# Performance work log

Measured on AMD Instinct MI355X. Metric: run time of the kernel, lower is better.

Reference implementation:

```python
import jax, jax.numpy as jnp
import numpy as np

IN_F = 1024
OUT_F = 1024
N_ORDER = 13  # grid_size=10 + spline_order=3
RMS_EPS = 1e-6


def setup_inputs() -> dict:
    key = jax.random.key(0)
    k_x, k_b, k_p = jax.random.split(key, 3)
    x = jax.random.normal(k_x, (4, 2048, IN_F), dtype=jnp.float32)
    # flax param init: normal(stddev=scale_base/sqrt(in_features)) etc.
    base_weight = jax.random.normal(k_b, (IN_F, OUT_F), dtype=jnp.float32) * (1.0 / np.sqrt(IN_F))
    poly_weight = jax.random.normal(k_p, (N_ORDER, IN_F, OUT_F), dtype=jnp.float32) * (0.1 / np.sqrt(IN_F * N_ORDER))
    rms_scale = jnp.ones((OUT_F,), dtype=jnp.float32)  # nn.RMSNorm default scale init
    return {"x": x, "base_weight": base_weight, "poly_weight": poly_weight, "rms_scale": rms_scale}


def reference(x, base_weight, poly_weight, rms_scale):
    orig_dtype = x.dtype
    prefix = x.shape[:-1]
    x_2d = x.reshape(-1, IN_F)  # [B, in]

    # Base path: SiLU(x) @ W_base in bf16
    x_c = x_2d.astype(jnp.bfloat16)
    out = jax.nn.silu(x_c) @ base_weight.astype(jnp.bfloat16)  # [B, out] bf16

    # Chebyshev recursion on tanh-normalized fp32 input
    x_safe = jnp.tanh(x_2d.astype(jnp.float32))
    pw = poly_weight.astype(jnp.bfloat16)
    T_prev = jnp.ones_like(x_safe)
    T_curr = x_safe
    out = out + T_prev.astype(jnp.bfloat16) @ pw[0]
    out = out + T_curr.astype(jnp.bfloat16) @ pw[1]
    for k in range(2, N_ORDER):  # fixed small unroll (13 orders)
        T_next = 2.0 * x_safe * T_curr - T_prev
        out = out + T_next.astype(jnp.bfloat16) @ pw[k]
        T_prev = T_curr
        T_curr = T_next

    # RMSNorm (flax default: eps=1e-6, learned scale)
    o32 = out.astype(jnp.float32)
    ms = jnp.mean(o32 * o32, axis=-1, keepdims=True)
    o32 = o32 * jax.lax.rsqrt(ms + RMS_EPS) * rms_scale
    return o32.astype(orig_dtype).reshape(prefix + (OUT_F,))
```

## Files before the change

kernel.cpp:

```cpp
#include <hip/hip_runtime.h>
#include <cstdint>

#define IN_F  1024
#define OUT_F 1024
#define NORD  13
#define BROWS 8192

typedef __bf16 bf16x8 __attribute__((ext_vector_type(8)));
typedef float  f32x4  __attribute__((ext_vector_type(4)));
typedef unsigned short u16x8 __attribute__((ext_vector_type(8)));
typedef unsigned short u16x4 __attribute__((ext_vector_type(4)));

__device__ __forceinline__ unsigned short f2bf(float f) {
  unsigned int u = __float_as_uint(f);
  unsigned int r = u + 0x7FFFu + ((u >> 16) & 1u);
  return (unsigned short)(r >> 16);
}
__device__ __forceinline__ float bf2f(unsigned short h) {
  return __uint_as_float(((unsigned int)h) << 16);
}
__device__ __forceinline__ float bfround(float f) { return bf2f(f2bf(f)); }

__device__ __forceinline__ void gload_lds16(const void* g, void* l) {
  __builtin_amdgcn_global_load_lds(
      (__attribute__((address_space(1))) unsigned int*)(uintptr_t)g,
      (__attribute__((address_space(3))) unsigned int*)(unsigned int)(uintptr_t)l,
      16, 0, 0);
}

__global__ __launch_bounds__(256)
void act_kernel(const float* __restrict__ x, unsigned short* __restrict__ A,
                int b0, int nb, int Kp) {
  int t   = threadIdx.x;
  int row = blockIdx.x * 2 + (t >> 7);
  int f0  = (t & 127) * 8;
  const float* xr = x + (size_t)row * IN_F + f0;
  float xv[8];
  *(float4*)&xv[0] = *(const float4*)&xr[0];
  *(float4*)&xv[4] = *(const float4*)&xr[4];
  unsigned short* Ar = A + (size_t)row * Kp;
  int omax = b0 + nb - 1;
  if (b0 == 0) {
    u16x8 sv;
#pragma unroll
    for (int i = 0; i < 8; i++) {
      float xc = bfround(xv[i]);
      float sg = bfround(1.0f / (1.0f + expf(-xc)));
      sv[i] = f2bf(xc * sg);
    }
    *(u16x8*)&Ar[f0] = sv;
  }
  float xs[8], tp[8], tc[8];
#pragma unroll
  for (int i = 0; i < 8; i++) { xs[i] = tanhf(xv[i]); tp[i] = 1.0f; tc[i] = xs[i]; }
  for (int o = 1; o <= omax; o++) {
    if (o >= b0) {
      int bb = o - b0;
      u16x8 sv;
#pragma unroll
      for (int i = 0; i < 8; i++) sv[i] = f2bf(tc[i]);
      *(u16x8*)&Ar[(size_t)bb * 1024 + f0] = sv;
    }
    {
#pragma clang fp contract(off)
#pragma unroll
      for (int i = 0; i < 8; i++) {
        float tm = 2.0f * xs[i] * tc[i];
        float tn = tm - tp[i];
        tp[i] = tc[i]; tc[i] = tn;
      }
    }
  }
}

__global__ __launch_bounds__(256)
void wprep_kernel(const float* __restrict__ baseW, const float* __restrict__ poly,
                  unsigned short* __restrict__ Wt, int b0, int Kp) {
  __shared__ float tile[64][65];
  int bb = blockIdx.z;
  int g  = b0 + bb;
  const float* src = (g == 0) ? baseW : (poly + (size_t)g * (IN_F * OUT_F));
  int n0 = blockIdx.x * 64, f0 = blockIdx.y * 64;
  int tx = threadIdx.x, ty = threadIdx.y;
#pragma unroll
  for (int i = 0; i < 16; i++)
    tile[ty + i * 4][tx] = src[(size_t)(f0 + ty + i * 4) * OUT_F + n0 + tx];
  __syncthreads();
#pragma unroll
  for (int i = 0; i < 16; i++)
    Wt[(size_t)(n0 + ty + i * 4) * Kp + (size_t)bb * 1024 + f0 + tx] = f2bf(tile[tx][ty + i * 4]);
}

__global__ __launch_bounds__(256)
void bias1_kernel(const float* __restrict__ pw0, float* __restrict__ partial) {
  int t  = threadIdx.x;
  int n  = blockIdx.x * 256 + t;
  int fc = blockIdx.y;
  float s = 0.f;
  for (int f = fc * 128; f < fc * 128 + 128; f++)
    s += bf2f(f2bf(pw0[(size_t)f * OUT_F + n]));
  partial[(size_t)fc * OUT_F + n] = s;
}
__global__ __launch_bounds__(256)
void bias2_kernel(const float* __restrict__ partial, float* __restrict__ bias) {
  int n = blockIdx.x * 256 + threadIdx.x;
  float s = 0.f;
#pragma unroll
  for (int fc = 0; fc < 8; fc++) s += partial[(size_t)fc * OUT_F + n];
  bias[n] = s;
}

__global__ __launch_bounds__(256, 2)
void gemm_kernel(const unsigned short* __restrict__ A, const unsigned short* __restrict__ Wt,
                 unsigned short* __restrict__ outAcc, const float* __restrict__ bias,
                 int Kp, int isFirst) {
  __shared__ unsigned short sA[2][128 * 64];
  __shared__ unsigned short sB[2][128 * 64];
  int t    = threadIdx.x;
  int m0   = blockIdx.x * 128;
  int n0   = blockIdx.y * 128;
  int wave = t >> 6, lane = t & 63;
  int lr   = lane & 15, quad = lane >> 4;
  int wm   = (wave & 1) * 64, wn = (wave >> 1) * 64;

  int rs = t >> 3;
  int jg = (t & 7) ^ (rs & 7);
  const unsigned short* aSrc = A  + (size_t)(m0 + rs) * Kp + jg * 8;
  const unsigned short* bSrc = Wt + (size_t)(n0 + rs) * Kp + jg * 8;
  char* sAc = (char*)sA;
  char* sBc = (char*)sB;
  int ldsOff = t * 16;

  int aOff[4][2], bOff[4][2];
#pragma unroll
  for (int mi = 0; mi < 4; mi++) {
    int row = wm + mi * 16 + lr;
#pragma unroll
    for (int ks = 0; ks < 2; ks++) {
      int j = ks * 4 + quad;
      aOff[mi][ks] = row * 128 + ((j ^ (row & 7)) * 16);
    }
  }
#pragma unroll
  for (int ni = 0; ni < 4; ni++) {
    int row = wn + ni * 16 + lr;
#pragma unroll
    for (int ks = 0; ks < 2; ks++) {
      int j = ks * 4 + quad;
      bOff[ni][ks] = row * 128 + ((j ^ (row & 7)) * 16);
    }
  }

  f32x4 s[4][4];
  float bsr[4];
  if (isFirst) {
#pragma unroll
    for (int ni = 0; ni < 4; ni++) bsr[ni] = bfround(bias[n0 + wn + ni * 16 + lr]);
  } else {
#pragma unroll
    for (int ni = 0; ni < 4; ni++) {
      int gn = n0 + wn + ni * 16 + lr;
#pragma unroll
      for (int mi = 0; mi < 4; mi++) {
        int gmBase = m0 + wm + mi * 16 + quad * 4;
#pragma unroll
        for (int r = 0; r < 4; r++)
          s[mi][ni][r] = bf2f(outAcc[(size_t)(gmBase + r) * OUT_F + gn]);
      }
    }
  }

  int nKt  = Kp >> 6;
  int nBlk = Kp >> 10;

  auto stage = [&](int gkt, int buf) {
    const unsigned short* aP = aSrc + gkt * 64;
    const unsigned short* bP = bSrc + gkt * 64;
    char* dA = sAc + buf * 16384 + ldsOff;
    char* dB = sBc + buf * 16384 + ldsOff;
#pragma unroll
    for (int rd = 0; rd < 4; rd++)
      gload_lds16(aP + (size_t)rd * 32 * Kp, dA + rd * 4096);
#pragma unroll
    for (int rd = 0; rd < 4; rd++)
      gload_lds16(bP + (size_t)rd * 32 * Kp, dB + rd * 4096);
  };

  stage(0, 0);

  int gkt = 0;
  for (int blk = 0; blk < nBlk; blk++) {
    f32x4 acc[4][4];
#pragma unroll
    for (int mi = 0; mi < 4; mi++)
#pragma unroll
      for (int ni = 0; ni < 4; ni++)
        acc[mi][ni] = (f32x4){0.f, 0.f, 0.f, 0.f};

    for (int kt = 0; kt < 16; kt++, gkt++) {
      __syncthreads();
      int nxt = gkt + 1;
      if (nxt < nKt) stage(nxt, nxt & 1);
      int buf = gkt & 1;
      char* bA = sAc + buf * 16384;
      char* bB = sBc + buf * 16384;
#pragma unroll
      for (int ks = 0; ks < 2; ks++) {
        bf16x8 af[4], bfr[4];
#pragma unroll
        for (int mi = 0; mi < 4; mi++) af[mi] = *(const bf16x8*)(bA + aOff[mi][ks]);
#pragma unroll
        for (int ni = 0; ni < 4; ni++) bfr[ni] = *(const bf16x8*)(bB + bOff[ni][ks]);
#pragma unroll
        for (int mi = 0; mi < 4; mi++)
#pragma unroll
          for (int ni = 0; ni < 4; ni++)
            acc[mi][ni] = __builtin_amdgcn_mfma_f32_16x16x32_bf16(af[mi], bfr[ni], acc[mi][ni], 0, 0, 0);
      }
    }

    bool firstBlk = (isFirst && blk == 0);
    if (firstBlk) {
#pragma unroll
      for (int mi = 0; mi < 4; mi++)
#pragma unroll
        for (int ni = 0; ni < 4; ni++)
#pragma unroll
          for (int r = 0; r < 4; r++) {
            float p = bfround(acc[mi][ni][r]);
            s[mi][ni][r] = bfround(p + bsr[ni]);
          }
    } else {
#pragma unroll
      for (int mi = 0; mi < 4; mi++)
#pragma unroll
        for (int ni = 0; ni < 4; ni++)
#pragma unroll
          for (int r = 0; r < 4; r++)
            s[mi][ni][r] = bfround(s[mi][ni][r] + bfround(acc[mi][ni][r]));
    }
  }

#pragma unroll
  for (int ni = 0; ni < 4; ni++) {
    int gn = n0 + wn + ni * 16 + lr;
#pragma unroll
    for (int mi = 0; mi < 4; mi++) {
      int gmBase = m0 + wm + mi * 16 + quad * 4;
#pragma unroll
      for (int r = 0; r < 4; r++)
        outAcc[(size_t)(gmBase + r) * OUT_F + gn] = f2bf(s[mi][ni][r]);
    }
  }
}

__global__ __launch_bounds__(256)
void rms_kernel(const unsigned short* __restrict__ outAcc, const float* __restrict__ scale,
                float* __restrict__ out) {
  int row = blockIdx.x;
  int t   = threadIdx.x;
  const unsigned short* src = outAcc + (size_t)row * OUT_F;
  u16x4 hv = *(const u16x4*)&src[t * 4];
  float v[4];
#pragma unroll
  for (int i = 0; i < 4; i++) v[i] = bf2f(hv[i]);
  float s = v[0]*v[0] + v[1]*v[1] + v[2]*v[2] + v[3]*v[3];
#pragma unroll
  for (int off = 32; off > 0; off >>= 1) s += __shfl_down(s, off, 64);
  __shared__ float red[4];
  if ((t & 63) == 0) red[t >> 6] = s;
  __syncthreads();
  float tot = red[0] + red[1] + red[2] + red[3];
  float sc = 1.0f / sqrtf(tot * (1.0f / OUT_F) + 1e-6f);
  float4 so = *(const float4*)&scale[t * 4];
  float4 o;
  o.x = v[0] * sc * so.x; o.y = v[1] * sc * so.y;
  o.z = v[2] * sc * so.z; o.w = v[3] * sc * so.w;
  *(float4*)&out[(size_t)row * OUT_F + t * 4] = o;
}

extern "C" void kernel_launch(void* const* d_in, const int* in_sizes, int n_in,
                              void* d_out, int out_size, void* d_ws, size_t ws_size,
                              hipStream_t stream) {
  const float* x     = (const float*)d_in[0];
  const float* baseW = (const float*)d_in[1];
  const float* poly  = (const float*)d_in[2];
  const float* scale = (const float*)d_in[3];
  float* out = (float*)d_out;

  char* ws = (char*)d_ws;
  unsigned short* outAcc = (unsigned short*)ws;
  float* bias    = (float*)(ws + 16777216);
  float* partial = (float*)(ws + 16777216 + 4096);
  size_t fixed   = 16777216 + 4096 + 32768;

  int CHB = 1;
  for (int c = NORD; c >= 1; c--) {
    size_t need = fixed + (size_t)c * 1024 * OUT_F * 2
                + (size_t)BROWS * c * 1024 * 2;
    if (need <= ws_size) { CHB = c; break; }
  }
  unsigned short* Wt = (unsigned short*)(ws + fixed);
  unsigned short* Ap = (unsigned short*)(ws + fixed + (size_t)CHB * 1024 * OUT_F * 2);

  bias1_kernel<<<dim3(4, 8), 256, 0, stream>>>(poly, partial);
  bias2_kernel<<<4, 256, 0, stream>>>(partial, bias);

  for (int b0 = 0; b0 < NORD; b0 += CHB) {
    int nb = (CHB < NORD - b0) ? CHB : (NORD - b0);
    int Kp = nb * 1024;
    act_kernel<<<BROWS / 2, 256, 0, stream>>>(x, Ap, b0, nb, Kp);
    wprep_kernel<<<dim3(16, 16, nb), dim3(64, 4), 0, stream>>>(baseW, poly, Wt, b0, Kp);
    gemm_kernel<<<dim3(BROWS / 128, 8), 256, 0, stream>>>(Ap, Wt, outAcc, bias, Kp, (b0 == 0) ? 1 : 0);
  }
  rms_kernel<<<BROWS, 256, 0, stream>>>(outAcc, scale, out);
}
```

Measured before the change: 407.0 us.

## Prefetch two K-tiles ahead with explicit vmcnt waits and swap to fast tanh/exp

```diff
diff --git a/kernel.cpp b/kernel.cpp
--- a/kernel.cpp
+++ b/kernel.cpp
@@ -20,6 +20,11 @@
   return __uint_as_float(((unsigned int)h) << 16);
 }
 __device__ __forceinline__ float bfround(float f) { return bf2f(f2bf(f)); }
+
+__device__ __forceinline__ float fast_tanh(float x) {
+  float e = __expf(2.0f * x);
+  return 1.0f - 2.0f / (e + 1.0f);
+}
 
 __device__ __forceinline__ void gload_lds16(const void* g, void* l) {
   __builtin_amdgcn_global_load_lds(
@@ -45,14 +50,14 @@
 #pragma unroll
     for (int i = 0; i < 8; i++) {
       float xc = bfround(xv[i]);
-      float sg = bfround(1.0f / (1.0f + expf(-xc)));
+      float sg = bfround(1.0f / (1.0f + __expf(-xc)));
       sv[i] = f2bf(xc * sg);
     }
     *(u16x8*)&Ar[f0] = sv;
   }
   float xs[8], tp[8], tc[8];
 #pragma unroll
-  for (int i = 0; i < 8; i++) { xs[i] = tanhf(xv[i]); tp[i] = 1.0f; tc[i] = xs[i]; }
+  for (int i = 0; i < 8; i++) { xs[i] = fast_tanh(xv[i]); tp[i] = 1.0f; tc[i] = xs[i]; }
   for (int o = 1; o <= omax; o++) {
     if (o >= b0) {
       int bb = o - b0;
@@ -187,8 +192,10 @@
   };
 
   stage(0, 0);
-
-  int gkt = 0;
+  stage(1, 1);
+
+  int gkt   = 0;
+  int nKtm1 = nKt - 1;
   for (int blk = 0; blk < nBlk; blk++) {
     f32x4 acc[4][4];
 #pragma unroll
@@ -198,25 +205,39 @@
         acc[mi][ni] = (f32x4){0.f, 0.f, 0.f, 0.f};
 
     for (int kt = 0; kt < 16; kt++, gkt++) {
-      __syncthreads();
-      int nxt = gkt + 1;
-      if (nxt < nKt) stage(nxt, nxt & 1);
+      if (gkt != nKtm1) {
+        asm volatile("s_waitcnt vmcnt(8)" ::: "memory");
+      } else {
+        asm volatile("s_waitcnt vmcnt(0)" ::: "memory");
+      }
+      __builtin_amdgcn_s_barrier();
+      __builtin_amdgcn_sched_barrier(0);
+
       int buf = gkt & 1;
       char* bA = sAc + buf * 16384;
       char* bB = sBc + buf * 16384;
+      bf16x8 af[2][4], bfr[2][4];
 #pragma unroll
       for (int ks = 0; ks < 2; ks++) {
-        bf16x8 af[4], bfr[4];
-#pragma unroll
-        for (int mi = 0; mi < 4; mi++) af[mi] = *(const bf16x8*)(bA + aOff[mi][ks]);
-#pragma unroll
-        for (int ni = 0; ni < 4; ni++) bfr[ni] = *(const bf16x8*)(bB + bOff[ni][ks]);
+#pragma unroll
+        for (int mi = 0; mi < 4; mi++) af[ks][mi] = *(const bf16x8*)(bA + aOff[mi][ks]);
+#pragma unroll
+        for (int ni = 0; ni < 4; ni++) bfr[ks][ni] = *(const bf16x8*)(bB + bOff[ni][ks]);
+      }
+      asm volatile("s_waitcnt lgkmcnt(0)" ::: "memory");
+      __builtin_amdgcn_s_barrier();
+      __builtin_amdgcn_sched_barrier(0);
+
+      int nxt = gkt + 2;
+      if (nxt < nKt) stage(nxt, buf);
+
+#pragma unroll
+      for (int ks = 0; ks < 2; ks++)
 #pragma unroll
         for (int mi = 0; mi < 4; mi++)
 #pragma unroll
           for (int ni = 0; ni < 4; ni++)
-            acc[mi][ni] = __builtin_amdgcn_mfma_f32_16x16x32_bf16(af[mi], bfr[ni], acc[mi][ni], 0, 0, 0);
-      }
+            acc[mi][ni] = __builtin_amdgcn_mfma_f32_16x16x32_bf16(af[ks][mi], bfr[ks][ni], acc[mi][ni], 0, 0, 0);
     }
 
     bool firstBlk = (isFirst && blk == 0);
```

Result: slower. 431.9 us (+6.1%).

## Load GEMM A operand directly into registers, drop A LDS staging; fast tanh

Applied to the files above, without the earlier changes.

```diff
diff --git a/kernel.cpp b/kernel.cpp
--- a/kernel.cpp
+++ b/kernel.cpp
@@ -20,6 +20,11 @@
   return __uint_as_float(((unsigned int)h) << 16);
 }
 __device__ __forceinline__ float bfround(float f) { return bf2f(f2bf(f)); }
+
+__device__ __forceinline__ float fast_tanh(float x) {
+  float e = __expf(2.0f * x);
+  return 1.0f - 2.0f / (e + 1.0f);
+}
 
 __device__ __forceinline__ void gload_lds16(const void* g, void* l) {
   __builtin_amdgcn_global_load_lds(
@@ -45,14 +50,17 @@
 #pragma unroll
     for (int i = 0; i < 8; i++) {
       float xc = bfround(xv[i]);
-      float sg = bfround(1.0f / (1.0f + expf(-xc)));
+      float sg = bfround(1.0f / (1.0f + __expf(-xc)));
       sv[i] = f2bf(xc * sg);
     }
     *(u16x8*)&Ar[f0] = sv;
   }
-  float xs[8], tp[8], tc[8];
-#pragma unroll
-  for (int i = 0; i < 8; i++) { xs[i] = tanhf(xv[i]); tp[i] = 1.0f; tc[i] = xs[i]; }
+  float xs2[8], tp[8], tc[8];
+#pragma unroll
+  for (int i = 0; i < 8; i++) {
+    float xs = fast_tanh(xv[i]);
+    tp[i] = 1.0f; tc[i] = xs; xs2[i] = xs + xs;
+  }
   for (int o = 1; o <= omax; o++) {
     if (o >= b0) {
       int bb = o - b0;
@@ -65,7 +73,7 @@
 #pragma clang fp contract(off)
 #pragma unroll
       for (int i = 0; i < 8; i++) {
-        float tm = 2.0f * xs[i] * tc[i];
+        float tm = xs2[i] * tc[i];
         float tn = tm - tp[i];
         tp[i] = tc[i]; tc[i] = tn;
       }
@@ -114,7 +122,6 @@
 void gemm_kernel(const unsigned short* __restrict__ A, const unsigned short* __restrict__ Wt,
                  unsigned short* __restrict__ outAcc, const float* __restrict__ bias,
                  int Kp, int isFirst) {
-  __shared__ unsigned short sA[2][128 * 64];
   __shared__ unsigned short sB[2][128 * 64];
   int t    = threadIdx.x;
   int m0   = blockIdx.x * 128;
@@ -125,22 +132,11 @@
 
   int rs = t >> 3;
   int jg = (t & 7) ^ (rs & 7);
-  const unsigned short* aSrc = A  + (size_t)(m0 + rs) * Kp + jg * 8;
   const unsigned short* bSrc = Wt + (size_t)(n0 + rs) * Kp + jg * 8;
-  char* sAc = (char*)sA;
   char* sBc = (char*)sB;
   int ldsOff = t * 16;
 
-  int aOff[4][2], bOff[4][2];
-#pragma unroll
-  for (int mi = 0; mi < 4; mi++) {
-    int row = wm + mi * 16 + lr;
-#pragma unroll
-    for (int ks = 0; ks < 2; ks++) {
-      int j = ks * 4 + quad;
-      aOff[mi][ks] = row * 128 + ((j ^ (row & 7)) * 16);
-    }
-  }
+  int bOff[4][2];
 #pragma unroll
   for (int ni = 0; ni < 4; ni++) {
     int row = wn + ni * 16 + lr;
@@ -151,7 +147,9 @@
     }
   }
 
-  f32x4 s[4][4];
+  const unsigned short* aBase = A + (size_t)(m0 + wm + lr) * Kp + quad * 8;
+
+  unsigned short sp[4][4][4];
   float bsr[4];
   if (isFirst) {
 #pragma unroll
@@ -165,7 +163,7 @@
         int gmBase = m0 + wm + mi * 16 + quad * 4;
 #pragma unroll
         for (int r = 0; r < 4; r++)
-          s[mi][ni][r] = bf2f(outAcc[(size_t)(gmBase + r) * OUT_F + gn]);
+          sp[mi][ni][r] = outAcc[(size_t)(gmBase + r) * OUT_F + gn];
       }
     }
   }
@@ -173,50 +171,66 @@
   int nKt  = Kp >> 6;
   int nBlk = Kp >> 10;
 
-  auto stage = [&](int gkt, int buf) {
-    const unsigned short* aP = aSrc + gkt * 64;
+  auto stageB = [&](int gkt, int buf) {
     const unsigned short* bP = bSrc + gkt * 64;
-    char* dA = sAc + buf * 16384 + ldsOff;
     char* dB = sBc + buf * 16384 + ldsOff;
-#pragma unroll
-    for (int rd = 0; rd < 4; rd++)
-      gload_lds16(aP + (size_t)rd * 32 * Kp, dA + rd * 4096);
 #pragma unroll
     for (int rd = 0; rd < 4; rd++)
       gload_lds16(bP + (size_t)rd * 32 * Kp, dB + rd * 4096);
   };
 
-  stage(0, 0);
-
+  auto loadA = [&](int gkt, bf16x8 (&ar)[4][2]) {
+    const unsigned short* p = aBase + (size_t)gkt * 64;
+#pragma unroll
+    for (int mi = 0; mi < 4; mi++)
+#pragma unroll
+      for (int ks = 0; ks < 2; ks++)
+        ar[mi][ks] = *(const bf16x8*)(p + (size_t)mi * 16 * Kp + ks * 32);
+  };
+
+  bf16x8 arP[4][2], arQ[4][2];
+
+  stageB(0, 0);
+  loadA(0, arP);
+
+  f32x4 acc[4][4];
   int gkt = 0;
+
+  auto ktStep = [&](const bf16x8 (&arC)[4][2], bf16x8 (&arN)[4][2]) {
+    __syncthreads();
+    int nxt = gkt + 1;
+    int buf = gkt & 1;
+    if (nxt < nKt) {
+      stageB(nxt, buf ^ 1);
+      loadA(nxt, arN);
+    }
+    char* bB = sBc + buf * 16384;
+    bf16x8 bfv[2][4];
+#pragma unroll
+    for (int ks = 0; ks < 2; ks++)
+#pragma unroll
+      for (int ni = 0; ni < 4; ni++)
+        bfv[ks][ni] = *(const bf16x8*)(bB + bOff[ni][ks]);
+#pragma unroll
+    for (int ks = 0; ks < 2; ks++)
+#pragma unroll
+      for (int mi = 0; mi < 4; mi++)
+#pragma unroll
+        for (int ni = 0; ni < 4; ni++)
+          acc[mi][ni] = __builtin_amdgcn_mfma_f32_16x16x32_bf16(arC[mi][ks], bfv[ks][ni], acc[mi][ni], 0, 0, 0);
+    gkt++;
+  };
+
   for (int blk = 0; blk < nBlk; blk++) {
-    f32x4 acc[4][4];
 #pragma unroll
     for (int mi = 0; mi < 4; mi++)
 #pragma unroll
       for (int ni = 0; ni < 4; ni++)
         acc[mi][ni] = (f32x4){0.f, 0.f, 0.f, 0.f};
 
-    for (int kt = 0; kt < 16; kt++, gkt++) {
-      __syncthreads();
-      int nxt = gkt + 1;
-      if (nxt < nKt) stage(nxt, nxt & 1);
-      int buf = gkt & 1;
-      char* bA = sAc + buf * 16384;
-      char* bB = sBc + buf * 16384;
-#pragma unroll
-      for (int ks = 0; ks < 2; ks++) {
-        bf16x8 af[4], bfr[4];
-#pragma unroll
-        for (int mi = 0; mi < 4; mi++) af[mi] = *(const bf16x8*)(bA + aOff[mi][ks]);
-#pragma unroll
-        for (int ni = 0; ni < 4; ni++) bfr[ni] = *(const bf16x8*)(bB + bOff[ni][ks]);
-#pragma unroll
-        for (int mi = 0; mi < 4; mi++)
-#pragma unroll
-          for (int ni = 0; ni < 4; ni++)
-            acc[mi][ni] = __builtin_amdgcn_mfma_f32_16x16x32_bf16(af[mi], bfr[ni], acc[mi][ni], 0, 0, 0);
-      }
+    for (int kt2 = 0; kt2 < 8; kt2++) {
+      ktStep(arP, arQ);
+      ktStep(arQ, arP);
     }
 
     bool firstBlk = (isFirst && blk == 0);
@@ -228,7 +242,7 @@
 #pragma unroll
           for (int r = 0; r < 4; r++) {
             float p = bfround(acc[mi][ni][r]);
-            s[mi][ni][r] = bfround(p + bsr[ni]);
+            sp[mi][ni][r] = f2bf(p + bsr[ni]);
           }
     } else {
 #pragma unroll
@@ -237,7 +251,7 @@
         for (int ni = 0; ni < 4; ni++)
 #pragma unroll
           for (int r = 0; r < 4; r++)
-            s[mi][ni][r] = bfround(s[mi][ni][r] + bfround(acc[mi][ni][r]));
+            sp[mi][ni][r] = f2bf(bf2f(sp[mi][ni][r]) + bfround(acc[mi][ni][r]));
     }
   }
 
@@ -249,7 +263,7 @@
       int gmBase = m0 + wm + mi * 16 + quad * 4;
 #pragma unroll
       for (int r = 0; r < 4; r++)
-        outAcc[(size_t)(gmBase + r) * OUT_F + gn] = f2bf(s[mi][ni][r]);
+        outAcc[(size_t)(gmBase + r) * OUT_F + gn] = sp[mi][ni][r];
     }
   }
 }
```

New measurement: 621.6 us. +52.7%, slower.

## Use two-wave GEMM blocks with larger per-wave tiles and fast tanh/exp

Applied to the files above, without the earlier changes.

```diff
diff --git a/kernel.cpp b/kernel.cpp
--- a/kernel.cpp
+++ b/kernel.cpp
@@ -20,6 +20,11 @@
   return __uint_as_float(((unsigned int)h) << 16);
 }
 __device__ __forceinline__ float bfround(float f) { return bf2f(f2bf(f)); }
+
+__device__ __forceinline__ float fast_tanh(float x) {
+  float e = __expf(2.0f * x);
+  return 1.0f - 2.0f / (e + 1.0f);
+}
 
 __device__ __forceinline__ void gload_lds16(const void* g, void* l) {
   __builtin_amdgcn_global_load_lds(
@@ -45,14 +50,17 @@
 #pragma unroll
     for (int i = 0; i < 8; i++) {
       float xc = bfround(xv[i]);
-      float sg = bfround(1.0f / (1.0f + expf(-xc)));
+      float sg = bfround(1.0f / (1.0f + __expf(-xc)));
       sv[i] = f2bf(xc * sg);
     }
     *(u16x8*)&Ar[f0] = sv;
   }
-  float xs[8], tp[8], tc[8];
-#pragma unroll
-  for (int i = 0; i < 8; i++) { xs[i] = tanhf(xv[i]); tp[i] = 1.0f; tc[i] = xs[i]; }
+  float xs2[8], tp[8], tc[8];
+#pragma unroll
+  for (int i = 0; i < 8; i++) {
+    float xs = fast_tanh(xv[i]);
+    tp[i] = 1.0f; tc[i] = xs; xs2[i] = xs + xs;
+  }
   for (int o = 1; o <= omax; o++) {
     if (o >= b0) {
       int bb = o - b0;
@@ -65,7 +73,7 @@
 #pragma clang fp contract(off)
 #pragma unroll
       for (int i = 0; i < 8; i++) {
-        float tm = 2.0f * xs[i] * tc[i];
+        float tm = xs2[i] * tc[i];
         float tn = tm - tp[i];
         tp[i] = tc[i]; tc[i] = tn;
       }
@@ -110,7 +118,7 @@
   bias[n] = s;
 }
 
-__global__ __launch_bounds__(256, 2)
+__global__ __launch_bounds__(128, 1)
 void gemm_kernel(const unsigned short* __restrict__ A, const unsigned short* __restrict__ Wt,
                  unsigned short* __restrict__ outAcc, const float* __restrict__ bias,
                  int Kp, int isFirst) {
@@ -121,7 +129,7 @@
   int n0   = blockIdx.y * 128;
   int wave = t >> 6, lane = t & 63;
   int lr   = lane & 15, quad = lane >> 4;
-  int wm   = (wave & 1) * 64, wn = (wave >> 1) * 64;
+  int wn   = wave * 64;
 
   int rs = t >> 3;
   int jg = (t & 7) ^ (rs & 7);
@@ -131,10 +139,10 @@
   char* sBc = (char*)sB;
   int ldsOff = t * 16;
 
-  int aOff[4][2], bOff[4][2];
-#pragma unroll
-  for (int mi = 0; mi < 4; mi++) {
-    int row = wm + mi * 16 + lr;
+  int aOff[8][2], bOff[4][2];
+#pragma unroll
+  for (int mi = 0; mi < 8; mi++) {
+    int row = mi * 16 + lr;
 #pragma unroll
     for (int ks = 0; ks < 2; ks++) {
       int j = ks * 4 + quad;
@@ -151,7 +159,7 @@
     }
   }
 
-  f32x4 s[4][4];
+  unsigned short sp[8][4][4];
   float bsr[4];
   if (isFirst) {
 #pragma unroll
@@ -161,11 +169,11 @@
     for (int ni = 0; ni < 4; ni++) {
       int gn = n0 + wn + ni * 16 + lr;
 #pragma unroll
-      for (int mi = 0; mi < 4; mi++) {
-        int gmBase = m0 + wm + mi * 16 + quad * 4;
+      for (int mi = 0; mi < 8; mi++) {
+        int gmBase = m0 + mi * 16 + quad * 4;
 #pragma unroll
         for (int r = 0; r < 4; r++)
-          s[mi][ni][r] = bf2f(outAcc[(size_t)(gmBase + r) * OUT_F + gn]);
+          sp[mi][ni][r] = outAcc[(size_t)(gmBase + r) * OUT_F + gn];
       }
     }
   }
@@ -173,26 +181,26 @@
   int nKt  = Kp >> 6;
   int nBlk = Kp >> 10;
 
-  auto stage = [&](int gkt, int buf) {
-    const unsigned short* aP = aSrc + gkt * 64;
-    const unsigned short* bP = bSrc + gkt * 64;
+  auto stage = [&](int g, int buf) {
+    const unsigned short* aP = aSrc + (size_t)g * 64;
+    const unsigned short* bP = bSrc + (size_t)g * 64;
     char* dA = sAc + buf * 16384 + ldsOff;
     char* dB = sBc + buf * 16384 + ldsOff;
 #pragma unroll
-    for (int rd = 0; rd < 4; rd++)
-      gload_lds16(aP + (size_t)rd * 32 * Kp, dA + rd * 4096);
-#pragma unroll
-    for (int rd = 0; rd < 4; rd++)
-      gload_lds16(bP + (size_t)rd * 32 * Kp, dB + rd * 4096);
+    for (int rd = 0; rd < 8; rd++)
+      gload_lds16(aP + (size_t)rd * 16 * Kp, dA + rd * 2048);
+#pragma unroll
+    for (int rd = 0; rd < 8; rd++)
+      gload_lds16(bP + (size_t)rd * 16 * Kp, dB + rd * 2048);
   };
 
   stage(0, 0);
 
   int gkt = 0;
   for (int blk = 0; blk < nBlk; blk++) {
-    f32x4 acc[4][4];
-#pragma unroll
-    for (int mi = 0; mi < 4; mi++)
+    f32x4 acc[8][4];
+#pragma unroll
+    for (int mi = 0; mi < 8; mi++)
 #pragma unroll
       for (int ni = 0; ni < 4; ni++)
         acc[mi][ni] = (f32x4){0.f, 0.f, 0.f, 0.f};
@@ -202,17 +210,17 @@
       int nxt = gkt + 1;
       if (nxt < nKt) stage(nxt, nxt & 1);
       int buf = gkt & 1;
-      char* bA = sAc + buf * 16384;
-      char* bB = sBc + buf * 16384;
+      const char* bA = sAc + buf * 16384;
+      const char* bB = sBc + buf * 16384;
 #pragma unroll
       for (int ks = 0; ks < 2; ks++) {
-        bf16x8 af[4], bfr[4];
-#pragma unroll
-        for (int mi = 0; mi < 4; mi++) af[mi] = *(const bf16x8*)(bA + aOff[mi][ks]);
+        bf16x8 af[8], bfr[4];
+#pragma unroll
+        for (int mi = 0; mi < 8; mi++) af[mi] = *(const bf16x8*)(bA + aOff[mi][ks]);
 #pragma unroll
         for (int ni = 0; ni < 4; ni++) bfr[ni] = *(const bf16x8*)(bB + bOff[ni][ks]);
 #pragma unroll
-        for (int mi = 0; mi < 4; mi++)
+        for (int mi = 0; mi < 8; mi++)
 #pragma unroll
           for (int ni = 0; ni < 4; ni++)
             acc[mi][ni] = __builtin_amdgcn_mfma_f32_16x16x32_bf16(af[mi], bfr[ni], acc[mi][ni], 0, 0, 0);
@@ -222,22 +230,22 @@
     bool firstBlk = (isFirst && blk == 0);
     if (firstBlk) {
 #pragma unroll
-      for (int mi = 0; mi < 4; mi++)
+      for (int mi = 0; mi < 8; mi++)
 #pragma unroll
         for (int ni = 0; ni < 4; ni++)
 #pragma unroll
           for (int r = 0; r < 4; r++) {
             float p = bfround(acc[mi][ni][r]);
-            s[mi][ni][r] = bfround(p + bsr[ni]);
+            sp[mi][ni][r] = f2bf(p + bsr[ni]);
           }
     } else {
 #pragma unroll
-      for (int mi = 0; mi < 4; mi++)
+      for (int mi = 0; mi < 8; mi++)
 #pragma unroll
         for (int ni = 0; ni < 4; ni++)
 #pragma unroll
           for (int r = 0; r < 4; r++)
-            s[mi][ni][r] = bfround(s[mi][ni][r] + bfround(acc[mi][ni][r]));
+            sp[mi][ni][r] = f2bf(bf2f(sp[mi][ni][r]) + bfround(acc[mi][ni][r]));
     }
   }
 
@@ -245,11 +253,11 @@
   for (int ni = 0; ni < 4; ni++) {
     int gn = n0 + wn + ni * 16 + lr;
 #pragma unroll
-    for (int mi = 0; mi < 4; mi++) {
-      int gmBase = m0 + wm + mi * 16 + quad * 4;
+    for (int mi = 0; mi < 8; mi++) {
+      int gmBase = m0 + mi * 16 + quad * 4;
 #pragma unroll
       for (int r = 0; r < 4; r++)
-        outAcc[(size_t)(gmBase + r) * OUT_F + gn] = f2bf(s[mi][ni][r]);
+        outAcc[(size_t)(gmBase + r) * OUT_F + gn] = sp[mi][ni][r];
     }
   }
 }
@@ -311,7 +319,7 @@
     int Kp = nb * 1024;
     act_kernel<<<BROWS / 2, 256, 0, stream>>>(x, Ap, b0, nb, Kp);
     wprep_kernel<<<dim3(16, 16, nb), dim3(64, 4), 0, stream>>>(baseW, poly, Wt, b0, Kp);
-    gemm_kernel<<<dim3(BROWS / 128, 8), 256, 0, stream>>>(Ap, Wt, outAcc, bias, Kp, (b0 == 0) ? 1 : 0);
+    gemm_kernel<<<dim3(BROWS / 128, 8), 128, 0, stream>>>(Ap, Wt, outAcc, bias, Kp, (b0 == 0) ? 1 : 0);
   }
   rms_kernel<<<BROWS, 256, 0, stream>>>(outAcc, scale, out);
 }
```

Measured after the change: 449.7 us. +10.5%, slower.
